# Kernel optimization log

Measured on AMD Instinct MI355X. Metric: run time of the kernel, lower is better.

## Reference

```python
import jax, jax.numpy as jnp
from jax import lax
import numpy as np

EPS = 1e-5  # BatchNorm eps (eval mode, fresh running stats: mean=0, var=1)

N, T, H, C = 16, 512, 64, 64
O, K, E = 64, 9, 256


def setup_inputs() -> dict:
    key = jax.random.key(0)
    ks = jax.random.split(key, 16)
    X = jax.random.normal(ks[0], (N, T, H, C), dtype=jnp.float32)
    edges = jax.random.randint(ks[1], (N, 2, E), 0, H, dtype=jnp.int64)
    # att1/att2: Conv2d(C,1,1) == dot over channels + bias
    w_att1 = jax.random.normal(ks[2], (C,), jnp.float32) * (1.0 / np.sqrt(C))
    b_att1 = jax.random.normal(ks[3], (), jnp.float32) * 0.01
    w_att2 = jax.random.normal(ks[4], (C,), jnp.float32) * (1.0 / np.sqrt(C))
    b_att2 = jax.random.normal(ks[5], (), jnp.float32) * 0.01
    # GCN linear
    W_lin = jax.random.normal(ks[6], (O, C), jnp.float32) * (1.0 / np.sqrt(C))
    b_lin = jax.random.normal(ks[7], (O,), jnp.float32) * 0.01
    # tcn: BN -> ReLU -> Conv2d(O,O,(K,1)) -> BN -> Dropout(eval=id)
    bn1_gamma = 1.0 + 0.1 * jax.random.normal(ks[8], (O,), jnp.float32)
    bn1_beta = 0.1 * jax.random.normal(ks[9], (O,), jnp.float32)
    W_tcn = jax.random.normal(ks[10], (O, O, K, 1), jnp.float32) * (1.0 / np.sqrt(O * K))
    b_tcn = jax.random.normal(ks[11], (O,), jnp.float32) * 0.01
    bn2_gamma = 1.0 + 0.1 * jax.random.normal(ks[12], (O,), jnp.float32)
    bn2_beta = 0.1 * jax.random.normal(ks[13], (O,), jnp.float32)
    return dict(X=X, edges=edges, w_att1=w_att1, b_att1=b_att1, w_att2=w_att2,
                b_att2=b_att2, W_lin=W_lin, b_lin=b_lin, bn1_gamma=bn1_gamma,
                bn1_beta=bn1_beta, W_tcn=W_tcn, b_tcn=b_tcn,
                bn2_gamma=bn2_gamma, bn2_beta=bn2_beta)


def _bn_eval(x, gamma, beta):
    # eval-mode BatchNorm2d with running_mean=0, running_var=1; x is (N, Cc, T, H)
    inv = gamma / jnp.sqrt(1.0 + EPS)
    return x * inv[None, :, None, None] + beta[None, :, None, None]


def _forward(X, edges, w_att1, b_att1, w_att2, b_att2, W_lin, b_lin,
             bn1_gamma, bn1_beta, W_tcn, b_tcn, bn2_gamma, bn2_beta):
    n, t, h, c = X.shape
    k = W_tcn.shape[2]
    # --- adjacency from edge lists (duplicates sum, as sparse_coo->to_dense) ---
    bidx = jnp.arange(n)[:, None]
    adj = jnp.zeros((n, h, h), X.dtype).at[bidx, edges[:, 0, :], edges[:, 1, :]].add(1.0)
    # --- attention: a1[n,t,h] + a2[n,t,h'], leaky_relu, softmax over h ---
    a1 = jnp.einsum('nthc,c->nth', X, w_att1) + b_att1
    a2 = jnp.einsum('nthc,c->nth', X, w_att2) + b_att2
    s = jax.nn.leaky_relu(a1[:, :, :, None] + a2[:, :, None, :], 0.01)  # (n,t,h,h')
    att = jax.nn.softmax(s, axis=2)  # softmax over h (dim=1 pre-permute)
    # --- GCN: einsum('nthh,ntho->ntho') only uses diag(adj@att + I) ---
    diag = jnp.einsum('nhk,ntkh->nth', adj, att) + 1.0
    support = jnp.einsum('nthc,oc->ntho', X, W_lin) + b_lin  # (n,t,h,O)
    g = diag[..., None] * support
    # --- tcn: BN -> ReLU -> temporal conv (K,1) -> BN -> Dropout(eval) ---
    y = jnp.transpose(g, (0, 3, 1, 2))  # (n,O,t,h)
    y = jax.nn.relu(_bn_eval(y, bn1_gamma, bn1_beta))
    pad = (k - 1) // 2
    y = lax.conv_general_dilated(y, W_tcn, window_strides=(1, 1),
                                 padding=[(pad, pad), (0, 0)])
    y = y + b_tcn[None, :, None, None]
    y = _bn_eval(y, bn2_gamma, bn2_beta)
    # --- residual (identity: in==out, stride=1) + relu ---
    y = y + jnp.transpose(X, (0, 3, 1, 2))
    return jnp.transpose(jax.nn.relu(y), (0, 2, 3, 1))  # (n,t,h,O)


def reference(X, edges, w_att1, b_att1, w_att2, b_att2, W_lin, b_lin,
              bn1_gamma, bn1_beta, W_tcn, b_tcn, bn2_gamma, bn2_beta):
    return _forward(X, edges, w_att1, b_att1, w_att2, b_att2, W_lin, b_lin,
                    bn1_gamma, bn1_beta, W_tcn, b_tcn, bn2_gamma, bn2_beta)
```

## Files before the change

kernel.cpp:

```cpp
#include <hip/hip_runtime.h>
#include <hip/hip_bf16.h>
#include <stdint.h>

typedef float f32x4 __attribute__((ext_vector_type(4)));
typedef __bf16 bf16x8 __attribute__((ext_vector_type(8)));
typedef __bf16 bf16x4 __attribute__((ext_vector_type(4)));
typedef unsigned short u16;
typedef unsigned int u32;

__device__ __forceinline__ u16 f2bf(float f) {
    u32 u = __float_as_uint(f);
    u32 r = (u + 0x7fffu + ((u >> 16) & 1u)) >> 16;
    return (u16)r;
}

#define NB_ATTN 2048

__global__ __launch_bounds__(256) void k_attn(
    const float* __restrict__ X, const int* __restrict__ edges,
    const float* __restrict__ w1g, const float* __restrict__ b1g,
    const float* __restrict__ w2g, const float* __restrict__ b2g,
    const float* __restrict__ Wlin, const float* __restrict__ Wtcn,
    u16* __restrict__ wlin_p, u16* __restrict__ wtcn_p,
    float* __restrict__ diag) {
    const int tid = threadIdx.x;
    const int bid = blockIdx.x;

    if (bid >= NB_ATTN) {
        int idx = (bid - NB_ATTN) * 256 + tid;
        if (idx < 4096) {
            int jj = idx & 7, l = (idx >> 3) & 63, j = (idx >> 9) & 3, s = idx >> 11;
            int o = j * 16 + (l & 15);
            int c = s * 32 + (l >> 4) * 8 + jj;
            wlin_p[idx] = f2bf(Wlin[o * 64 + c]);
        }
        int i2 = idx - 4096;
        if (i2 >= 0 && i2 < 36864) {
            int jj = i2 & 7, l = (i2 >> 3) & 63, j = (i2 >> 9) & 3, s = (i2 >> 11) & 1, kk = i2 >> 12;
            int o = j * 16 + (l & 15);
            int op = s * 32 + (l >> 4) * 8 + jj;
            wtcn_p[i2] = f2bf(Wtcn[(o * 64 + op) * 9 + kk]);
        }
        return;
    }

    __shared__ __align__(16) float adjs[64 * 65];
    __shared__ float wl[128];

    const int n = bid >> 7;
    const int t = (bid & 127) * 4 + (tid >> 6);
    const int h = tid & 63;

    {
        f32x4 z4 = {0.f, 0.f, 0.f, 0.f};
        for (int i = tid; i < 1040; i += 256) *(f32x4*)(&adjs[i * 4]) = z4;
    }
    if (tid < 128) wl[tid] = (tid < 64) ? w1g[tid] : w2g[tid - 64];
    __syncthreads();
    {
        int r = edges[n * 512 + tid];
        int c = edges[n * 512 + 256 + tid];
        atomicAdd(&adjs[r * 65 + c], 1.0f);
    }
    __syncthreads();

    const float* Xr = X + ((size_t)(n * 512 + t) * 64 + h) * 64;
    float a1 = b1g[0], a2 = b2g[0];
#pragma unroll 4
    for (int c4 = 0; c4 < 16; c4++) {
        float4 xv = *(const float4*)(Xr + c4 * 4);
        float4 w1v = *(const float4*)(&wl[c4 * 4]);
        float4 w2v = *(const float4*)(&wl[64 + c4 * 4]);
        a1 += xv.x * w1v.x + xv.y * w1v.y + xv.z * w1v.z + xv.w * w1v.w;
        a2 += xv.x * w2v.x + xv.y * w2v.y + xv.z * w2v.z + xv.w * w2v.w;
    }

    float num = 0.f, den = 0.f;
    const float* arow = &adjs[h * 65];
#pragma unroll
    for (int k = 0; k < 64; k++) {
        float s = __shfl(a1, k) + a2;
        s = fmaxf(s, 0.01f * s);
        float e = __expf(s);
        den += e;
        num = fmaf(arow[k], e, num);
    }
    diag[((size_t)(n * 64 + h)) * 512 + t] = num / den + 1.0f;
}

__global__ __launch_bounds__(256) void k_gcn_tcn(
    const float* __restrict__ X, const float* __restrict__ diag,
    const u16* __restrict__ wlin_p, const float* __restrict__ blin,
    const float* __restrict__ g1, const float* __restrict__ be1,
    const u16* __restrict__ wtcn_p, const float* __restrict__ btcn,
    const float* __restrict__ g2, const float* __restrict__ be2,
    float* __restrict__ out) {
    __shared__ __align__(16) u16 As[144 * 72];

    const int tid = threadIdx.x;
    const int bid = blockIdx.x;
    const int n = bid >> 8, h = (bid >> 2) & 63, tb = (bid & 3) * 128;
    const float* Xbase = X + ((size_t)(n * 512) * 64 + h) * 64;
    const float* diagb = diag + ((size_t)(n * 64 + h)) * 512;

    const int w = tid >> 6, l = tid & 63;
    const int col = l & 15, q = l >> 4;
    const float rsf = 1.0f / sqrtf(1.0f + 1e-5f);
    const f32x4 zv = {0.f, 0.f, 0.f, 0.f};

    for (int mt = w; mt < 9; mt += 4) {
#pragma unroll
        for (int i = 0; i < 4; i++) {
            int idx = l + 64 * i;
            int r = 16 * mt + (idx >> 4), c4 = idx & 15;
            int tg = tb - 4 + r;
            float4 xv = make_float4(0.f, 0.f, 0.f, 0.f);
            if (tg >= 0 && tg < 512) xv = *(const float4*)(Xbase + (size_t)tg * 4096 + c4 * 4);
            bf16x4 pk;
            pk[0] = (__bf16)xv.x; pk[1] = (__bf16)xv.y;
            pk[2] = (__bf16)xv.z; pk[3] = (__bf16)xv.w;
            *(bf16x4*)(&As[r * 72 + c4 * 4]) = pk;
        }
        float dg[4];
#pragma unroll
        for (int rr = 0; rr < 4; rr++) {
            int tg = tb - 4 + 16 * mt + q * 4 + rr;
            dg[rr] = (tg >= 0 && tg < 512) ? diagb[tg] : 0.f;
        }
        f32x4 acc[4] = {zv, zv, zv, zv};
#pragma unroll
        for (int s = 0; s < 2; s++) {
            bf16x8 a = *(const bf16x8*)(&As[(16 * mt + col) * 72 + s * 32 + q * 8]);
#pragma unroll
            for (int j = 0; j < 4; j++) {
                bf16x8 b = *(const bf16x8*)(&wlin_p[((s * 4 + j) * 64 + l) * 8]);
                acc[j] = __builtin_amdgcn_mfma_f32_16x16x32_bf16(a, b, acc[j], 0, 0, 0);
            }
        }
#pragma unroll
        for (int j = 0; j < 4; j++) {
            int o = 16 * j + col;
            float s1 = g1[o] * rsf;
            float bb = be1[o];
            float bl = blin[o];
#pragma unroll
            for (int rr = 0; rr < 4; rr++) {
                int row = 16 * mt + q * 4 + rr;
                int tg = tb - 4 + row;
                float v = (acc[j][rr] + bl) * dg[rr] * s1 + bb;
                v = v > 0.f ? v : 0.f;
                if (tg < 0 || tg >= 512) v = 0.f;
                __bf16 bv = (__bf16)v;
                As[row * 72 + o] = __builtin_bit_cast(u16, bv);
            }
        }
    }
    __syncthreads();

    f32x4 acc2[2][4];
#pragma unroll
    for (int mt = 0; mt < 2; mt++)
#pragma unroll
        for (int j = 0; j < 4; j++) acc2[mt][j] = zv;

    for (int kk = 0; kk < 9; kk++) {
#pragma unroll
        for (int s = 0; s < 2; s++) {
            bf16x8 b[4];
#pragma unroll
            for (int j = 0; j < 4; j++)
                b[j] = *(const bf16x8*)(&wtcn_p[(((kk * 2 + s) * 4 + j) * 64 + l) * 8]);
            bf16x8 a[2];
#pragma unroll
            for (int mt = 0; mt < 2; mt++) {
                int row = 32 * w + 16 * mt + col + kk;
                a[mt] = *(const bf16x8*)(&As[row * 72 + s * 32 + q * 8]);
            }
#pragma unroll
            for (int mt = 0; mt < 2; mt++)
#pragma unroll
                for (int j = 0; j < 4; j++)
                    acc2[mt][j] = __builtin_amdgcn_mfma_f32_16x16x32_bf16(a[mt], b[j], acc2[mt][j], 0, 0, 0);
        }
    }

    float s2[4], c2[4];
#pragma unroll
    for (int j = 0; j < 4; j++) {
        int o = 16 * j + col;
        float s = g2[o] * rsf;
        s2[j] = s;
        c2[j] = btcn[o] * s + be2[o];
    }
#pragma unroll
    for (int mt = 0; mt < 2; mt++) {
#pragma unroll
        for (int rr = 0; rr < 4; rr++) {
            int tt = tb + 32 * w + 16 * mt + 4 * q + rr;
#pragma unroll
            for (int j = 0; j < 4; j++) {
                int o = 16 * j + col;
                size_t off = ((size_t)(n * 512 + tt) * 64 + h) * 64 + o;
                float v = acc2[mt][j][rr] * s2[j] + c2[j] + X[off];
                out[off] = v > 0.f ? v : 0.f;
            }
        }
    }
}

extern "C" void kernel_launch(void* const* d_in, const int* in_sizes, int n_in,
                              void* d_out, int out_size, void* d_ws, size_t ws_size,
                              hipStream_t stream) {
    const float* X    = (const float*)d_in[0];
    const int*  edges = (const int*)d_in[1];
    const float* w1   = (const float*)d_in[2];
    const float* b1   = (const float*)d_in[3];
    const float* w2   = (const float*)d_in[4];
    const float* b2   = (const float*)d_in[5];
    const float* Wlin = (const float*)d_in[6];
    const float* blin = (const float*)d_in[7];
    const float* g1   = (const float*)d_in[8];
    const float* be1  = (const float*)d_in[9];
    const float* Wtcn = (const float*)d_in[10];
    const float* btcn = (const float*)d_in[11];
    const float* g2   = (const float*)d_in[12];
    const float* be2  = (const float*)d_in[13];
    float* out = (float*)d_out;

    char* ws = (char*)d_ws;
    u16*   wlin_p = (u16*)ws;
    u16*   wtcn_p = (u16*)(ws + 8192);
    float* diag   = (float*)(ws + 8192 + 73728);

    hipLaunchKernelGGL(k_attn, dim3(NB_ATTN + 160), dim3(256), 0, stream,
                       X, edges, w1, b1, w2, b2, Wlin, Wtcn, wlin_p, wtcn_p, diag);
    hipLaunchKernelGGL(k_gcn_tcn, dim3(16 * 64 * 4), dim3(256), 0, stream,
                       X, diag, wlin_p, blin, g1, be1, wtcn_p, btcn, g2, be2, out);
}
```

Measured before the change: 335.3 us.

## Coalesce attention X loads with shuffle reductions and stage GCN tile upfront

The attention kernel now has each wave read one time step's full H×C slab as contiguous float4s instead of one strided row per lane. Per-node dot products are reduced with cross-lane xor shuffles, staged through shared memory, and paired with a transposed adjacency so the softmax-weighted sum reads conflict-free columns. The GCN/TCN kernel now loads the whole 144-row X tile and its diag values into shared memory in one prologue before the MFMA loop, replacing per-wave interleaved loads. This adds shuffle instructions and an extra shared buffer in exchange for better global memory coalescing.

```diff
diff --git a/kernel.cpp b/kernel.cpp
--- a/kernel.cpp
+++ b/kernel.cpp
@@ -44,48 +44,61 @@
         return;
     }
 
-    __shared__ __align__(16) float adjs[64 * 65];
-    __shared__ float wl[128];
+    __shared__ __align__(16) float adjT[64 * 65];
+    __shared__ __align__(16) float A1s[4][64], A2s[4][64];
 
     const int n = bid >> 7;
-    const int t = (bid & 127) * 4 + (tid >> 6);
-    const int h = tid & 63;
+    const int tg = bid & 127;
+    const int w = tid >> 6, l = tid & 63;
+    const int t = tg * 4 + w;
+    const int c4 = l & 15, q = l >> 4;
 
     {
         f32x4 z4 = {0.f, 0.f, 0.f, 0.f};
-        for (int i = tid; i < 1040; i += 256) *(f32x4*)(&adjs[i * 4]) = z4;
-    }
-    if (tid < 128) wl[tid] = (tid < 64) ? w1g[tid] : w2g[tid - 64];
+        for (int i = tid; i < 1040; i += 256) *(f32x4*)(&adjT[i * 4]) = z4;
+    }
     __syncthreads();
     {
         int r = edges[n * 512 + tid];
         int c = edges[n * 512 + 256 + tid];
-        atomicAdd(&adjs[r * 65 + c], 1.0f);
-    }
-    __syncthreads();
-
-    const float* Xr = X + ((size_t)(n * 512 + t) * 64 + h) * 64;
-    float a1 = b1g[0], a2 = b2g[0];
-#pragma unroll 4
-    for (int c4 = 0; c4 < 16; c4++) {
-        float4 xv = *(const float4*)(Xr + c4 * 4);
-        float4 w1v = *(const float4*)(&wl[c4 * 4]);
-        float4 w2v = *(const float4*)(&wl[64 + c4 * 4]);
-        a1 += xv.x * w1v.x + xv.y * w1v.y + xv.z * w1v.z + xv.w * w1v.w;
-        a2 += xv.x * w2v.x + xv.y * w2v.y + xv.z * w2v.z + xv.w * w2v.w;
-    }
-
-    float num = 0.f, den = 0.f;
-    const float* arow = &adjs[h * 65];
-#pragma unroll
-    for (int k = 0; k < 64; k++) {
-        float s = __shfl(a1, k) + a2;
-        s = fmaxf(s, 0.01f * s);
-        float e = __expf(s);
-        den += e;
-        num = fmaf(arow[k], e, num);
-    }
-    diag[((size_t)(n * 64 + h)) * 512 + t] = num / den + 1.0f;
+        atomicAdd(&adjT[c * 65 + r], 1.0f);
+    }
+
+    const float* Xt = X + (size_t)(n * 512 + t) * 4096;
+    const float4 w1v = *(const float4*)(w1g + c4 * 4);
+    const float4 w2v = *(const float4*)(w2g + c4 * 4);
+    float a1h = 0.f, a2h = 0.f;
+#pragma unroll 8
+    for (int i = 0; i < 16; i++) {
+        float4 xv = *(const float4*)(Xt + (i * 64 + l) * 4);
+        float p1 = xv.x * w1v.x + xv.y * w1v.y + xv.z * w1v.z + xv.w * w1v.w;
+        float p2 = xv.x * w2v.x + xv.y * w2v.y + xv.z * w2v.z + xv.w * w2v.w;
+        p1 += __shfl_xor(p1, 1); p1 += __shfl_xor(p1, 2);
+        p1 += __shfl_xor(p1, 4); p1 += __shfl_xor(p1, 8);
+        p2 += __shfl_xor(p2, 1); p2 += __shfl_xor(p2, 2);
+        p2 += __shfl_xor(p2, 4); p2 += __shfl_xor(p2, 8);
+        if (c4 == i) { a1h = p1; a2h = p2; }
+    }
+    {
+        int hh = c4 * 4 + q;
+        A1s[w][hh] = a1h + b1g[0];
+        A2s[w][hh] = a2h + b2g[0];
+    }
+    __syncthreads();
+
+    {
+        float a2 = A2s[w][l];
+        float num = 0.f, den = 0.f;
+#pragma unroll 16
+        for (int k = 0; k < 64; k++) {
+            float s = A1s[w][k] + a2;
+            s = fmaxf(s, 0.01f * s);
+            float e = __expf(s);
+            den += e;
+            num = fmaf(adjT[k * 65 + l], e, num);
+        }
+        diag[((size_t)(n * 64 + l)) * 512 + t] = num / den + 1.0f;
+    }
 }
 
 __global__ __launch_bounds__(256) void k_gcn_tcn(
@@ -96,12 +109,30 @@
     const float* __restrict__ g2, const float* __restrict__ be2,
     float* __restrict__ out) {
     __shared__ __align__(16) u16 As[144 * 72];
+    __shared__ float DGs[144];
 
     const int tid = threadIdx.x;
     const int bid = blockIdx.x;
     const int n = bid >> 8, h = (bid >> 2) & 63, tb = (bid & 3) * 128;
     const float* Xbase = X + ((size_t)(n * 512) * 64 + h) * 64;
-    const float* diagb = diag + ((size_t)(n * 64 + h)) * 512;
+
+#pragma unroll
+    for (int i = 0; i < 9; i++) {
+        int idx = tid + 256 * i;
+        int r = idx >> 4, c4 = idx & 15;
+        int tg = tb - 4 + r;
+        float4 xv = make_float4(0.f, 0.f, 0.f, 0.f);
+        if (tg >= 0 && tg < 512) xv = *(const float4*)(Xbase + (size_t)tg * 4096 + c4 * 4);
+        bf16x4 pk;
+        pk[0] = (__bf16)xv.x; pk[1] = (__bf16)xv.y;
+        pk[2] = (__bf16)xv.z; pk[3] = (__bf16)xv.w;
+        *(bf16x4*)(&As[r * 72 + c4 * 4]) = pk;
+    }
+    if (tid < 144) {
+        int tg = tb - 4 + tid;
+        DGs[tid] = (tg >= 0 && tg < 512) ? diag[((size_t)(n * 64 + h)) * 512 + tg] : 0.f;
+    }
+    __syncthreads();
 
     const int w = tid >> 6, l = tid & 63;
     const int col = l & 15, q = l >> 4;
@@ -109,24 +140,6 @@
     const f32x4 zv = {0.f, 0.f, 0.f, 0.f};
 
     for (int mt = w; mt < 9; mt += 4) {
-#pragma unroll
-        for (int i = 0; i < 4; i++) {
-            int idx = l + 64 * i;
-            int r = 16 * mt + (idx >> 4), c4 = idx & 15;
-            int tg = tb - 4 + r;
-            float4 xv = make_float4(0.f, 0.f, 0.f, 0.f);
-            if (tg >= 0 && tg < 512) xv = *(const float4*)(Xbase + (size_t)tg * 4096 + c4 * 4);
-            bf16x4 pk;
-            pk[0] = (__bf16)xv.x; pk[1] = (__bf16)xv.y;
-            pk[2] = (__bf16)xv.z; pk[3] = (__bf16)xv.w;
-            *(bf16x4*)(&As[r * 72 + c4 * 4]) = pk;
-        }
-        float dg[4];
-#pragma unroll
-        for (int rr = 0; rr < 4; rr++) {
-            int tg = tb - 4 + 16 * mt + q * 4 + rr;
-            dg[rr] = (tg >= 0 && tg < 512) ? diagb[tg] : 0.f;
-        }
         f32x4 acc[4] = {zv, zv, zv, zv};
 #pragma unroll
         for (int s = 0; s < 2; s++) {
@@ -147,7 +160,7 @@
             for (int rr = 0; rr < 4; rr++) {
                 int row = 16 * mt + q * 4 + rr;
                 int tg = tb - 4 + row;
-                float v = (acc[j][rr] + bl) * dg[rr] * s1 + bb;
+                float v = (acc[j][rr] + bl) * DGs[row] * s1 + bb;
                 v = v > 0.f ? v : 0.f;
                 if (tg < 0 || tg >= 512) v = 0.f;
                 __bf16 bv = (__bf16)v;
```

After: 321.3 us. -4.2%, faster.
